# Performance work log

Measured on AMD Instinct MI355X. Metric: run time of the kernel, lower is better.

Reference implementation:

```python
import jax, jax.numpy as jnp
import numpy as np

B, D, H, W, C = 2, 5, 32, 32, 256
NH, NL, NP = 8, 5, 16
HD = C // NH
MLP_H = 4 * C
HW = H * W
LQ = D * HW


def setup_inputs() -> dict:
    key = jax.random.key(0)
    ks = jax.random.split(key, 12)
    s = 0.02
    return {
        "x": jax.random.normal(ks[0], (B, D, H, W, C), jnp.float32),
        "reference_points": jax.random.uniform(ks[1], (B, LQ, NL, 2), jnp.float32),
        "spatial_shapes": np.array([[H, W]] * NL, np.int32),
        "level_start_index": (np.arange(NL) * HW).astype(np.int32),
        "norm3_g": jnp.ones((C,), jnp.float32),
        "norm3_b": jnp.zeros((C,), jnp.float32),
        "norm4_g": jnp.ones((C,), jnp.float32),
        "norm4_b": jnp.zeros((C,), jnp.float32),
        "w_off": jax.random.normal(ks[2], (C, NH * NL * NP * 2), jnp.float32) * s,
        "b_off": jnp.zeros((NH * NL * NP * 2,), jnp.float32),
        "w_attn": jax.random.normal(ks[3], (C, NH * NL * NP), jnp.float32) * s,
        "b_attn": jnp.zeros((NH * NL * NP,), jnp.float32),
        "w_val": jax.random.normal(ks[4], (C, C), jnp.float32) * s,
        "b_val": jnp.zeros((C,), jnp.float32),
        "w_out": jax.random.normal(ks[5], (C, C), jnp.float32) * s,
        "b_out": jnp.zeros((C,), jnp.float32),
        "w_fc1": jax.random.normal(ks[6], (C, MLP_H), jnp.float32) * s,
        "b_fc1": jnp.zeros((MLP_H,), jnp.float32),
        "w_fc2": jax.random.normal(ks[7], (MLP_H, C), jnp.float32) * s,
        "b_fc2": jnp.zeros((C,), jnp.float32),
    }


def _ln(x, g, b, eps=1e-5):
    m = x.mean(-1, keepdims=True)
    v = ((x - m) ** 2).mean(-1, keepdims=True)
    return (x - m) * jax.lax.rsqrt(v + eps) * g + b


def _msdeform(q, ref, w_off, b_off, w_attn, b_attn, w_val, b_val, w_out, b_out):
    """Standard Deformable-DETR MSDeformAttn; self-attention (value = query input)."""
    Bq = q.shape[0]
    val = (q @ w_val + b_val).reshape(Bq, LQ, NH, HD)
    off = (q @ w_off + b_off).reshape(Bq, LQ, NH, NL, NP, 2)
    aw = jax.nn.softmax((q @ w_attn + b_attn).reshape(Bq, LQ, NH, NL * NP), axis=-1)
    aw = aw.reshape(Bq, LQ, NH, NL, NP)
    # offset normalizer: (W, H) per level (all levels HxW here)
    loc = ref[:, :, None, :, None, :] + off / jnp.array([W, H], jnp.float32)
    out = jnp.zeros((Bq, LQ, NH, HD), jnp.float32)
    for l in range(NL):  # loop over 5 levels (structural, small)
        vl = val[:, l * HW:(l + 1) * HW].transpose(0, 2, 1, 3).reshape(Bq * NH, HW, HD)
        ll = loc[:, :, :, l].transpose(0, 2, 1, 3, 4)  # [B, NH, LQ, NP, 2]
        # grid_sample align_corners=False, grid = 2*loc - 1 => pixel = loc*size - 0.5
        px = ll[..., 0] * W - 0.5
        py = ll[..., 1] * H - 0.5
        x0 = jnp.floor(px)
        y0 = jnp.floor(py)
        fx = px - x0
        fy = py - y0
        x0i = x0.astype(jnp.int32)
        y0i = y0.astype(jnp.int32)
        samp = jnp.zeros((Bq * NH, LQ * NP, HD), jnp.float32)
        for dy, dx, wgt in ((0, 0, (1 - fy) * (1 - fx)), (0, 1, (1 - fy) * fx),
                            (1, 0, fy * (1 - fx)), (1, 1, fy * fx)):
            xi = x0i + dx
            yi = y0i + dy
            valid = ((xi >= 0) & (xi < W) & (yi >= 0) & (yi < H)).astype(jnp.float32)
            idx = (jnp.clip(yi, 0, H - 1) * W + jnp.clip(xi, 0, W - 1)).reshape(Bq * NH, LQ * NP, 1)
            g = jnp.take_along_axis(vl, idx, axis=1)  # [B*NH, LQ*NP, HD]
            samp = samp + g * (wgt * valid).reshape(Bq * NH, LQ * NP, 1)
        samp = samp.reshape(Bq, NH, LQ, NP, HD)
        out = out + jnp.einsum('bqhp,bhqpd->bqhd', aw[:, :, :, l], samp)
    return out.reshape(Bq, LQ, C) @ w_out + b_out


def reference(x, reference_points, spatial_shapes, level_start_index,
              norm3_g, norm3_b, norm4_g, norm4_b,
              w_off, b_off, w_attn, b_attn, w_val, b_val, w_out, b_out,
              w_fc1, b_fc1, w_fc2, b_fc2):
    # forward_part3: norm3 -> flatten -> MSDeformAttn (D == 5, no padding path)
    q = _ln(x, norm3_g, norm3_b).reshape(B, LQ, C)
    attn = _msdeform(q, reference_points, w_off, b_off, w_attn, b_attn,
                     w_val, b_val, w_out, b_out)
    x = x + attn.reshape(B, D, H, W, C)  # shortcut + drop_path(identity)
    # forward_part4: norm4 -> MLP (GELU, exact) residual
    h = _ln(x, norm4_g, norm4_b)
    m = jax.nn.gelu(h @ w_fc1 + b_fc1, approximate=False) @ w_fc2 + b_fc2
    return x + m
```

## Files before the change

kernel.cpp:

```cpp
#include <hip/hip_runtime.h>
#include <hip/hip_bf16.h>
#include <math.h>

#define B_   2
#define D_   5
#define H_   32
#define W_   32
#define C_   256
#define NH_  8
#define NL_  5
#define NP_  16
#define HD_  32
#define HW_  1024
#define LQ_  5120
#define M_   (B_*LQ_)
#define MLP_ 1024
#define NCAT 2176

typedef unsigned short u16;
typedef __bf16 bf16x8 __attribute__((ext_vector_type(8)));
typedef float  f32x4  __attribute__((ext_vector_type(4)));
typedef float  f32x2  __attribute__((ext_vector_type(2)));

__device__ __forceinline__ float b2f(u16 v) {
    union { float f; unsigned u; } x; x.u = ((unsigned)v) << 16; return x.f;
}
__device__ __forceinline__ u16 f2b(float f) {
    union { float f; unsigned u; } x; x.f = f;
    unsigned r = x.u + 0x7fffu + ((x.u >> 16) & 1u);
    return (u16)(r >> 16);
}
__device__ __forceinline__ void gload16(const u16* g, u16* l) {
    __builtin_amdgcn_global_load_lds(
        (const __attribute__((address_space(1))) unsigned int*)g,
        (__attribute__((address_space(3))) unsigned int*)l, 16, 0, 0);
}

#define SEG0 557056
#define SEG1 622592
#define SEG2 884736
#define SEG3 1146880
#define SEGT 1149056
__global__ void prep_weights(const float* __restrict__ w_val, const float* __restrict__ w_off,
                             const float* __restrict__ w_attn, const float* __restrict__ w_out,
                             const float* __restrict__ w_fc1, const float* __restrict__ w_fc2,
                             const float* __restrict__ b_val, const float* __restrict__ b_off,
                             const float* __restrict__ b_attn,
                             u16* __restrict__ wcatT, u16* __restrict__ woutT,
                             u16* __restrict__ wfc1T, u16* __restrict__ wfc2T,
                             float* __restrict__ biascat) {
    int idx = blockIdx.x * blockDim.x + threadIdx.x;
    if (idx < SEG0) {
        int n = idx >> 8, k = idx & 255;
        float v;
        if (n < 256)        v = w_val[k * 256 + n];
        else if (n < 1536)  v = w_off[k * 1280 + (n - 256)];
        else                v = w_attn[k * 640 + (n - 1536)];
        wcatT[idx] = f2b(v);
    } else if (idx < SEG1) {
        int i = idx - SEG0; int n = i >> 8, k = i & 255;
        woutT[i] = f2b(w_out[k * 256 + n]);
    } else if (idx < SEG2) {
        int i = idx - SEG1; int n = i >> 8, k = i & 255;
        wfc1T[i] = f2b(w_fc1[k * 1024 + n]);
    } else if (idx < SEG3) {
        int i = idx - SEG2; int n = i >> 10, k = i & 1023;
        wfc2T[i] = f2b(w_fc2[k * 256 + n]);
    } else if (idx < SEGT) {
        int t = idx - SEG3;
        float v;
        if (t < 256)        v = b_val[t];
        else if (t < 1536)  v = b_off[t - 256];
        else                v = b_attn[t - 1536];
        biascat[t] = v;
    }
}

__global__ void ln_rows(const float* __restrict__ x, const float* __restrict__ g,
                        const float* __restrict__ b, u16* __restrict__ out) {
    int wave = threadIdx.x >> 6, lane = threadIdx.x & 63;
    int row = blockIdx.x * 4 + wave;
    const float4 v = *(const float4*)(x + (size_t)row * C_ + lane * 4);
    float s = v.x + v.y + v.z + v.w;
#pragma unroll
    for (int o = 1; o < 64; o <<= 1) s += __shfl_xor(s, o, 64);
    float mean = s * (1.0f / C_);
    float4 d = { v.x - mean, v.y - mean, v.z - mean, v.w - mean };
    float s2 = d.x * d.x + d.y * d.y + d.z * d.z + d.w * d.w;
#pragma unroll
    for (int o = 1; o < 64; o <<= 1) s2 += __shfl_xor(s2, o, 64);
    float r = rsqrtf(s2 * (1.0f / C_) + 1e-5f);
    const float4 gg = *(const float4*)(g + lane * 4);
    const float4 bb = *(const float4*)(b + lane * 4);
    unsigned lo = (unsigned)f2b(d.x * r * gg.x + bb.x) |
                  ((unsigned)f2b(d.y * r * gg.y + bb.y) << 16);
    unsigned hi = (unsigned)f2b(d.z * r * gg.z + bb.z) |
                  ((unsigned)f2b(d.w * r * gg.w + bb.w) << 16);
    uint2 pk = { lo, hi };
    *(uint2*)(out + (size_t)row * C_ + lane * 4) = pk;
}

#define BK 64
__launch_bounds__(256, 2)
__global__ void gemm128(const u16* __restrict__ A, const u16* __restrict__ Bt,
                        const float* __restrict__ bias,
                        void* __restrict__ out, int Mdim, int Ndim, int Kdim,
                        int mode, int nTiles) {
    __shared__ __align__(16) u16 lsA[128 * BK];
    __shared__ __align__(16) u16 lsB[128 * BK];
    int bm = blockIdx.x / nTiles, bn = blockIdx.x % nTiles;
    int m0 = bm * 128, n0 = bn * 128;
    int tid = threadIdx.x;
    int lane = tid & 63, wv = tid >> 6;
    int quad = lane >> 4, l16 = lane & 15;
    int rw = (wv >> 1) * 64, cw = (wv & 1) * 64;

    f32x4 acc[4][4];
#pragma unroll
    for (int i = 0; i < 4; i++)
#pragma unroll
        for (int j = 0; j < 4; j++) { f32x4 z = {0.f, 0.f, 0.f, 0.f}; acc[i][j] = z; }

    for (int k0 = 0; k0 < Kdim; k0 += BK) {
        __syncthreads();
#pragma unroll
        for (int s = 0; s < 4; s++) {
            int cc = s * 256 + wv * 64 + lane;
            int row = cc >> 3, kc = (cc & 7) << 3;
            int lbase = (s * 256 + wv * 64) * 8;
            gload16(A  + (size_t)(m0 + row) * Kdim + k0 + kc, &lsA[lbase]);
            gload16(Bt + (size_t)(n0 + row) * Kdim + k0 + kc, &lsB[lbase]);
        }
        __syncthreads();
#pragma unroll
        for (int kk = 0; kk < 2; kk++) {
            bf16x8 af[4], bfr[4];
#pragma unroll
            for (int i = 0; i < 4; i++)
                af[i] = *(const bf16x8*)(&lsA[(rw + i * 16 + l16) * BK + kk * 32 + quad * 8]);
#pragma unroll
            for (int j = 0; j < 4; j++)
                bfr[j] = *(const bf16x8*)(&lsB[(cw + j * 16 + l16) * BK + kk * 32 + quad * 8]);
#pragma unroll
            for (int i = 0; i < 4; i++)
#pragma unroll
                for (int j = 0; j < 4; j++)
                    acc[i][j] = __builtin_amdgcn_mfma_f32_16x16x32_bf16(
                        af[i], bfr[j], acc[i][j], 0, 0, 0);
        }
    }

#pragma unroll
    for (int i = 0; i < 4; i++) {
#pragma unroll
        for (int j = 0; j < 4; j++) {
            int col = n0 + cw + j * 16 + l16;
            float bb = bias[col];
#pragma unroll
            for (int r = 0; r < 4; r++) {
                int row = m0 + rw + i * 16 + quad * 4 + r;
                float v = acc[i][j][r] + bb;
                size_t off = (size_t)row * Ndim + col;
                if (mode == 0) {
                    ((u16*)out)[off] = f2b(v);
                } else {
                    float t = 0.5f * v * (1.0f + erff(v * 0.70710678f));
                    ((u16*)out)[off] = f2b(t);
                }
            }
        }
    }
}

__launch_bounds__(256, 4)
__global__ void gemm64_res(const u16* __restrict__ A, const u16* __restrict__ Bt,
                           const float* __restrict__ bias, const float* __restrict__ res,
                           float* __restrict__ out, int Mdim, int Ndim, int Kdim,
                           int nTiles) {
    __shared__ __align__(16) u16 lsA[64 * BK];
    __shared__ __align__(16) u16 lsB[128 * BK];
    int bm = blockIdx.x / nTiles, bn = blockIdx.x % nTiles;
    int m0 = bm * 64, n0 = bn * 128;
    int tid = threadIdx.x;
    int lane = tid & 63, wv = tid >> 6;
    int quad = lane >> 4, l16 = lane & 15;
    int rw = wv * 16;

    f32x4 acc[8];
#pragma unroll
    for (int j = 0; j < 8; j++) { f32x4 z = {0.f, 0.f, 0.f, 0.f}; acc[j] = z; }

    for (int k0 = 0; k0 < Kdim; k0 += BK) {
        __syncthreads();
#pragma unroll
        for (int s = 0; s < 2; s++) {
            int cc = s * 256 + wv * 64 + lane;
            int row = cc >> 3, kc = (cc & 7) << 3;
            int lbase = (s * 256 + wv * 64) * 8;
            gload16(A + (size_t)(m0 + row) * Kdim + k0 + kc, &lsA[lbase]);
        }
#pragma unroll
        for (int s = 0; s < 4; s++) {
            int cc = s * 256 + wv * 64 + lane;
            int row = cc >> 3, kc = (cc & 7) << 3;
            int lbase = (s * 256 + wv * 64) * 8;
            gload16(Bt + (size_t)(n0 + row) * Kdim + k0 + kc, &lsB[lbase]);
        }
        __syncthreads();
#pragma unroll
        for (int kk = 0; kk < 2; kk++) {
            bf16x8 af, bfr[8];
            af = *(const bf16x8*)(&lsA[(rw + l16) * BK + kk * 32 + quad * 8]);
#pragma unroll
            for (int j = 0; j < 8; j++)
                bfr[j] = *(const bf16x8*)(&lsB[(j * 16 + l16) * BK + kk * 32 + quad * 8]);
#pragma unroll
            for (int j = 0; j < 8; j++)
                acc[j] = __builtin_amdgcn_mfma_f32_16x16x32_bf16(
                    af, bfr[j], acc[j], 0, 0, 0);
        }
    }

#pragma unroll
    for (int j = 0; j < 8; j++) {
        int col = n0 + j * 16 + l16;
        float bb = bias[col];
#pragma unroll
        for (int r = 0; r < 4; r++) {
            int row = m0 + rw + quad * 4 + r;
            size_t off = (size_t)row * Ndim + col;
            out[off] = acc[j][r] + bb + res[off];
        }
    }
}

#define SPC 84
__launch_bounds__(256, 2)
__global__ void msdeform_sample(const u16* __restrict__ qkv,
                                const float* __restrict__ ref,
                                u16* __restrict__ outp) {
    __shared__ int2 sparam[NH_ * 4 * SPC];
    int m = blockIdx.x;
    int b = m / LQ_;
    int tid = threadIdx.x;
    int g = tid >> 5;
    int lane = tid & 31;

    const u16* logit_base = qkv + (size_t)m * NCAT + 1536 + g * 80;
    const u16* off_base   = qkv + (size_t)m * NCAT + 256  + g * 160;

    float lv[3];
    float lmax = -1e30f;
    {
        int c = 0;
        for (int i = lane; i < 80; i += 32, c++) {
            lv[c] = b2f(logit_base[i]);
            lmax = fmaxf(lmax, lv[c]);
        }
    }
#pragma unroll
    for (int o = 16; o > 0; o >>= 1) lmax = fmaxf(lmax, __shfl_xor(lmax, o, 32));
    float lsum = 0.f;
    {
        int c = 0;
        for (int i = lane; i < 80; i += 32, c++) {
            lv[c] = __expf(lv[c] - lmax);
            lsum += lv[c];
        }
    }
#pragma unroll
    for (int o = 16; o > 0; o >>= 1) lsum += __shfl_xor(lsum, o, 32);
    float inv = 1.0f / lsum;

    {
        int c = 0;
        for (int i = lane; i < 80; i += 32, c++) {
            float aw = lv[c] * inv;
            int l = i >> 4, p = i & 15;
            float rx = ref[((size_t)m * NL_ + l) * 2 + 0];
            float ry = ref[((size_t)m * NL_ + l) * 2 + 1];
            float ox = b2f(off_base[l * 32 + p * 2 + 0]);
            float oy = b2f(off_base[l * 32 + p * 2 + 1]);
            float px = rx * (float)W_ + ox - 0.5f;
            float py = ry * (float)H_ + oy - 0.5f;
            float x0 = floorf(px), y0 = floorf(py);
            float fx = px - x0, fy = py - y0;
            int x0i = (int)x0, y0i = (int)y0;
            int rowbase = b * LQ_ + l * HW_;
            int sbase = g * 4 * SPC + i;
#pragma unroll
            for (int cc = 0; cc < 4; cc++) {
                int dy = cc >> 1, dx = cc & 1;
                int xi = x0i + dx, yi = y0i + dy;
                float wgt = (dy ? fy : 1.f - fy) * (dx ? fx : 1.f - fx);
                bool valid = (xi >= 0) && (xi < W_) && (yi >= 0) && (yi < H_);
                int xc = min(max(xi, 0), W_ - 1);
                int yc = min(max(yi, 0), H_ - 1);
                int boff = (((rowbase + yc * W_ + xc) * NCAT) + g * 32) * 2;
                float w = valid ? wgt * aw : 0.f;
                int2 pk = { boff, __float_as_int(w) };
                sparam[sbase + cc * SPC] = pk;
            }
        }
    }
    __syncthreads();

    const char* qb = (const char*)qkv;
    int c4 = lane >> 3;
    int s2 = (lane >> 2) & 1;
    int chq = lane & 3;
    int pbase = g * 4 * SPC + c4 * SPC + s2;
    int laneoff = chq * 16;
    f32x2 p0 = {0.f, 0.f}, p1 = {0.f, 0.f}, p2 = {0.f, 0.f}, p3 = {0.f, 0.f};
#pragma unroll 8
    for (int i = 0; i < 40; i++) {
        int2 p = sparam[pbase + i * 2];
        f32x2 w2; w2.x = __int_as_float(p.y); w2.y = w2.x;
        unsigned voff = (unsigned)(p.x + laneoff);
        uint4 v = *(const uint4*)(qb + voff);
        union { unsigned u[2]; f32x2 f; } c0, c1, c2, c3;
        c0.u[0] = v.x << 16; c0.u[1] = v.x & 0xffff0000u;
        c1.u[0] = v.y << 16; c1.u[1] = v.y & 0xffff0000u;
        c2.u[0] = v.z << 16; c2.u[1] = v.z & 0xffff0000u;
        c3.u[0] = v.w << 16; c3.u[1] = v.w & 0xffff0000u;
        p0 += w2 * c0.f;
        p1 += w2 * c1.f;
        p2 += w2 * c2.f;
        p3 += w2 * c3.f;
    }
    float a0 = p0.x, a1 = p0.y, a2 = p1.x, a3 = p1.y;
    float a4 = p2.x, a5 = p2.y, a6 = p3.x, a7 = p3.y;
#pragma unroll
    for (int o = 4; o <= 16; o <<= 1) {
        a0 += __shfl_xor(a0, o, 32); a1 += __shfl_xor(a1, o, 32);
        a2 += __shfl_xor(a2, o, 32); a3 += __shfl_xor(a3, o, 32);
        a4 += __shfl_xor(a4, o, 32); a5 += __shfl_xor(a5, o, 32);
        a6 += __shfl_xor(a6, o, 32); a7 += __shfl_xor(a7, o, 32);
    }
    if (lane < 4) {
        uint4 pk;
        pk.x = (unsigned)f2b(a0) | ((unsigned)f2b(a1) << 16);
        pk.y = (unsigned)f2b(a2) | ((unsigned)f2b(a3) << 16);
        pk.z = (unsigned)f2b(a4) | ((unsigned)f2b(a5) << 16);
        pk.w = (unsigned)f2b(a6) | ((unsigned)f2b(a7) << 16);
        *(uint4*)(outp + (size_t)m * C_ + g * 32 + chq * 8) = pk;
    }
}

extern "C" void kernel_launch(void* const* d_in, const int* in_sizes, int n_in,
                              void* d_out, int out_size, void* d_ws, size_t ws_size,
                              hipStream_t stream) {
    const float* x      = (const float*)d_in[0];
    const float* ref    = (const float*)d_in[1];
    const float* n3g    = (const float*)d_in[4];
    const float* n3b    = (const float*)d_in[5];
    const float* n4g    = (const float*)d_in[6];
    const float* n4b    = (const float*)d_in[7];
    const float* w_off  = (const float*)d_in[8];
    const float* b_off  = (const float*)d_in[9];
    const float* w_attn = (const float*)d_in[10];
    const float* b_attn = (const float*)d_in[11];
    const float* w_val  = (const float*)d_in[12];
    const float* b_val  = (const float*)d_in[13];
    const float* w_out  = (const float*)d_in[14];
    const float* b_out  = (const float*)d_in[15];
    const float* w_fc1  = (const float*)d_in[16];
    const float* b_fc1  = (const float*)d_in[17];
    const float* w_fc2  = (const float*)d_in[18];
    const float* b_fc2  = (const float*)d_in[19];
    float* out = (float*)d_out;

    u16*   wcatT   = (u16*)d_ws;
    float* biascat = (float*)(wcatT + (size_t)NCAT * 256);
    u16*   woutT   = (u16*)(biascat + 2304);
    u16*   wfc1T   = woutT + 256 * 256;
    u16*   wfc2T   = wfc1T + 1024 * 256;
    u16*   qbuf    = wfc2T + 256 * 1024;
    u16*   qkv     = qbuf + (size_t)M_ * 256;
    u16*   outp    = qkv + (size_t)M_ * NCAT;
    float* x2      = (float*)qkv;
    u16*   hbuf    = (u16*)(x2 + (size_t)M_ * 256);
    u16*   gbuf    = hbuf + (size_t)M_ * 256;

    prep_weights<<<dim3((SEGT + 255) / 256), dim3(256), 0, stream>>>(
        w_val, w_off, w_attn, w_out, w_fc1, w_fc2, b_val, b_off, b_attn,
        wcatT, woutT, wfc1T, wfc2T, biascat);

    ln_rows<<<dim3(M_ / 4), dim3(256), 0, stream>>>(x, n3g, n3b, qbuf);

    gemm128<<<dim3(80 * 17), dim3(256), 0, stream>>>(
        qbuf, wcatT, biascat, qkv, M_, NCAT, 256, 0, 17);

    msdeform_sample<<<dim3(M_), dim3(256), 0, stream>>>(qkv, ref, outp);

    gemm64_res<<<dim3(160 * 2), dim3(256), 0, stream>>>(
        outp, woutT, b_out, x, x2, M_, 256, 256, 2);

    ln_rows<<<dim3(M_ / 4), dim3(256), 0, stream>>>(x2, n4g, n4b, hbuf);

    gemm128<<<dim3(80 * 8), dim3(256), 0, stream>>>(
        hbuf, wfc1T, b_fc1, gbuf, M_, 1024, 256, 1, 8);

    gemm64_res<<<dim3(160 * 2), dim3(256), 0, stream>>>(
        gbuf, wfc2T, b_fc2, x2, out, M_, 256, 1024, 2);
}
```

Baseline: 282.7 us.

## Store value projection head-major and fuse output projection with second LayerNorm

The fused projection GEMM now writes the value columns into a separate head-major buffer [B*NH, LQ, 32], so bilinear gathers in the sampling kernel read contiguous 64-byte rows instead of strided rows of the wide concatenated buffer. The remaining offset and logit columns go to a narrower buffer. A new kernel fuses the output projection, the residual add and the norm4 LayerNorm using a full-width 32-row tile, which removes one launch and a round trip of x2. The sampling inner loop is also rewritten with scalar accumulators and a smaller unroll. The cost is scattered epilogue stores in the GEMM and a single-pass variance formula in the fused LayerNorm.

```diff
diff --git a/kernel.cpp b/kernel.cpp
--- a/kernel.cpp
+++ b/kernel.cpp
@@ -16,11 +16,11 @@
 #define M_   (B_*LQ_)
 #define MLP_ 1024
 #define NCAT 2176
+#define NQ2  1920
 
 typedef unsigned short u16;
 typedef __bf16 bf16x8 __attribute__((ext_vector_type(8)));
 typedef float  f32x4  __attribute__((ext_vector_type(4)));
-typedef float  f32x2  __attribute__((ext_vector_type(2)));
 
 __device__ __forceinline__ float b2f(u16 v) {
     union { float f; unsigned u; } x; x.u = ((unsigned)v) << 16; return x.f;
@@ -104,7 +104,8 @@
 __launch_bounds__(256, 2)
 __global__ void gemm128(const u16* __restrict__ A, const u16* __restrict__ Bt,
                         const float* __restrict__ bias,
-                        void* __restrict__ out, int Mdim, int Ndim, int Kdim,
+                        u16* __restrict__ out, u16* __restrict__ valT,
+                        int Mdim, int Ndim, int Kdim,
                         int mode, int nTiles) {
     __shared__ __align__(16) u16 lsA[128 * BK];
     __shared__ __align__(16) u16 lsB[128 * BK];
@@ -160,15 +161,106 @@
             for (int r = 0; r < 4; r++) {
                 int row = m0 + rw + i * 16 + quad * 4 + r;
                 float v = acc[i][j][r] + bb;
-                size_t off = (size_t)row * Ndim + col;
                 if (mode == 0) {
-                    ((u16*)out)[off] = f2b(v);
+                    if (col < 256) {
+                        int b2 = row >= LQ_;
+                        int pix = row - b2 * LQ_;
+                        int h = col >> 5, ch = col & 31;
+                        valT[(((size_t)(b2 * NH_ + h) * LQ_) + pix) * 32 + ch] = f2b(v);
+                    } else {
+                        out[(size_t)row * NQ2 + (col - 256)] = f2b(v);
+                    }
                 } else {
                     float t = 0.5f * v * (1.0f + erff(v * 0.70710678f));
-                    ((u16*)out)[off] = f2b(t);
+                    out[(size_t)row * Ndim + col] = f2b(t);
                 }
             }
         }
+    }
+}
+
+__launch_bounds__(256, 2)
+__global__ void gemm_wout_ln(const u16* __restrict__ A, const u16* __restrict__ Bt,
+                             const float* __restrict__ bias, const float* __restrict__ res,
+                             const float* __restrict__ g4, const float* __restrict__ b4,
+                             float* __restrict__ x2, u16* __restrict__ hb) {
+    __shared__ __align__(16) u16 lsA[32 * BK];
+    __shared__ __align__(16) u16 lsB[256 * BK];
+    int m0 = blockIdx.x * 32;
+    int tid = threadIdx.x;
+    int lane = tid & 63, wv = tid >> 6;
+    int quad = lane >> 4, l16 = lane & 15;
+    int r0 = (wv & 1) * 16, c0 = (wv >> 1) * 128;
+
+    f32x4 acc[8];
+#pragma unroll
+    for (int j = 0; j < 8; j++) { f32x4 z = {0.f, 0.f, 0.f, 0.f}; acc[j] = z; }
+
+    for (int k0 = 0; k0 < 256; k0 += BK) {
+        __syncthreads();
+        {
+            int cc = wv * 64 + lane;
+            int row = cc >> 3, kc = (cc & 7) << 3;
+            gload16(A + (size_t)(m0 + row) * 256 + k0 + kc, &lsA[(wv * 64) * 8]);
+        }
+#pragma unroll
+        for (int s = 0; s < 8; s++) {
+            int cc = s * 256 + wv * 64 + lane;
+            int row = cc >> 3, kc = (cc & 7) << 3;
+            gload16(Bt + (size_t)row * 256 + k0 + kc, &lsB[(s * 256 + wv * 64) * 8]);
+        }
+        __syncthreads();
+#pragma unroll
+        for (int kk = 0; kk < 2; kk++) {
+            bf16x8 af, bfr[8];
+            af = *(const bf16x8*)(&lsA[(r0 + l16) * BK + kk * 32 + quad * 8]);
+#pragma unroll
+            for (int j = 0; j < 8; j++)
+                bfr[j] = *(const bf16x8*)(&lsB[(c0 + j * 16 + l16) * BK + kk * 32 + quad * 8]);
+#pragma unroll
+            for (int j = 0; j < 8; j++)
+                acc[j] = __builtin_amdgcn_mfma_f32_16x16x32_bf16(af, bfr[j], acc[j], 0, 0, 0);
+        }
+    }
+
+    __syncthreads();
+    float* tile = (float*)lsB;
+#pragma unroll
+    for (int j = 0; j < 8; j++) {
+        int col = c0 + j * 16 + l16;
+        float bb = bias[col];
+#pragma unroll
+        for (int r = 0; r < 4; r++) {
+            int rl = r0 + quad * 4 + r;
+            int row = m0 + rl;
+            float v = acc[j][r] + bb + res[(size_t)row * C_ + col];
+            tile[rl * 256 + col] = v;
+            x2[(size_t)row * C_ + col] = v;
+        }
+    }
+    __syncthreads();
+    const float4 gg = *(const float4*)(g4 + lane * 4);
+    const float4 bv = *(const float4*)(b4 + lane * 4);
+#pragma unroll
+    for (int rr = 0; rr < 8; rr++) {
+        int rl = wv * 8 + rr;
+        float4 v = *(const float4*)(&tile[rl * 256 + lane * 4]);
+        float s = v.x + v.y + v.z + v.w;
+        float s2 = v.x * v.x + v.y * v.y + v.z * v.z + v.w * v.w;
+#pragma unroll
+        for (int o = 1; o < 64; o <<= 1) {
+            s  += __shfl_xor(s, o, 64);
+            s2 += __shfl_xor(s2, o, 64);
+        }
+        float mean = s * (1.0f / C_);
+        float var = s2 * (1.0f / C_) - mean * mean;
+        float rstd = rsqrtf(var + 1e-5f);
+        unsigned lo = (unsigned)f2b((v.x - mean) * rstd * gg.x + bv.x) |
+                      ((unsigned)f2b((v.y - mean) * rstd * gg.y + bv.y) << 16);
+        unsigned hi = (unsigned)f2b((v.z - mean) * rstd * gg.z + bv.z) |
+                      ((unsigned)f2b((v.w - mean) * rstd * gg.w + bv.w) << 16);
+        uint2 pk = { lo, hi };
+        *(uint2*)(hb + (size_t)(m0 + rl) * C_ + lane * 4) = pk;
     }
 }
 
@@ -196,15 +288,13 @@
         for (int s = 0; s < 2; s++) {
             int cc = s * 256 + wv * 64 + lane;
             int row = cc >> 3, kc = (cc & 7) << 3;
-            int lbase = (s * 256 + wv * 64) * 8;
-            gload16(A + (size_t)(m0 + row) * Kdim + k0 + kc, &lsA[lbase]);
+            gload16(A + (size_t)(m0 + row) * Kdim + k0 + kc, &lsA[(s * 256 + wv * 64) * 8]);
         }
 #pragma unroll
         for (int s = 0; s < 4; s++) {
             int cc = s * 256 + wv * 64 + lane;
             int row = cc >> 3, kc = (cc & 7) << 3;
-            int lbase = (s * 256 + wv * 64) * 8;
-            gload16(Bt + (size_t)(n0 + row) * Kdim + k0 + kc, &lsB[lbase]);
+            gload16(Bt + (size_t)(n0 + row) * Kdim + k0 + kc, &lsB[(s * 256 + wv * 64) * 8]);
         }
         __syncthreads();
 #pragma unroll
@@ -216,8 +306,7 @@
                 bfr[j] = *(const bf16x8*)(&lsB[(j * 16 + l16) * BK + kk * 32 + quad * 8]);
 #pragma unroll
             for (int j = 0; j < 8; j++)
-                acc[j] = __builtin_amdgcn_mfma_f32_16x16x32_bf16(
-                    af, bfr[j], acc[j], 0, 0, 0);
+                acc[j] = __builtin_amdgcn_mfma_f32_16x16x32_bf16(af, bfr[j], acc[j], 0, 0, 0);
         }
     }
 
@@ -236,7 +325,8 @@
 
 #define SPC 84
 __launch_bounds__(256, 2)
-__global__ void msdeform_sample(const u16* __restrict__ qkv,
+__global__ void msdeform_sample(const u16* __restrict__ qkv2,
+                                const u16* __restrict__ valT,
                                 const float* __restrict__ ref,
                                 u16* __restrict__ outp) {
     __shared__ int2 sparam[NH_ * 4 * SPC];
@@ -246,8 +336,8 @@
     int g = tid >> 5;
     int lane = tid & 31;
 
-    const u16* logit_base = qkv + (size_t)m * NCAT + 1536 + g * 80;
-    const u16* off_base   = qkv + (size_t)m * NCAT + 256  + g * 160;
+    const u16* logit_base = qkv2 + (size_t)m * NQ2 + 1280 + g * 80;
+    const u16* off_base   = qkv2 + (size_t)m * NQ2 + g * 160;
 
     float lv[3];
     float lmax = -1e30f;
@@ -286,7 +376,7 @@
             float x0 = floorf(px), y0 = floorf(py);
             float fx = px - x0, fy = py - y0;
             int x0i = (int)x0, y0i = (int)y0;
-            int rowbase = b * LQ_ + l * HW_;
+            int hbase = (b * NH_ + g) * LQ_ + l * HW_;
             int sbase = g * 4 * SPC + i;
 #pragma unroll
             for (int cc = 0; cc < 4; cc++) {
@@ -296,7 +386,7 @@
                 bool valid = (xi >= 0) && (xi < W_) && (yi >= 0) && (yi < H_);
                 int xc = min(max(xi, 0), W_ - 1);
                 int yc = min(max(yi, 0), H_ - 1);
-                int boff = (((rowbase + yc * W_ + xc) * NCAT) + g * 32) * 2;
+                int boff = (hbase + yc * W_ + xc) * 64;
                 float w = valid ? wgt * aw : 0.f;
                 int2 pk = { boff, __float_as_int(w) };
                 sparam[sbase + cc * SPC] = pk;
@@ -305,31 +395,29 @@
     }
     __syncthreads();
 
-    const char* qb = (const char*)qkv;
+    const char* qb = (const char*)valT;
     int c4 = lane >> 3;
     int s2 = (lane >> 2) & 1;
     int chq = lane & 3;
     int pbase = g * 4 * SPC + c4 * SPC + s2;
     int laneoff = chq * 16;
-    f32x2 p0 = {0.f, 0.f}, p1 = {0.f, 0.f}, p2 = {0.f, 0.f}, p3 = {0.f, 0.f};
-#pragma unroll 8
+    float a0 = 0.f, a1 = 0.f, a2 = 0.f, a3 = 0.f;
+    float a4 = 0.f, a5 = 0.f, a6 = 0.f, a7 = 0.f;
+#pragma unroll 4
     for (int i = 0; i < 40; i++) {
         int2 p = sparam[pbase + i * 2];
-        f32x2 w2; w2.x = __int_as_float(p.y); w2.y = w2.x;
-        unsigned voff = (unsigned)(p.x + laneoff);
-        uint4 v = *(const uint4*)(qb + voff);
-        union { unsigned u[2]; f32x2 f; } c0, c1, c2, c3;
-        c0.u[0] = v.x << 16; c0.u[1] = v.x & 0xffff0000u;
-        c1.u[0] = v.y << 16; c1.u[1] = v.y & 0xffff0000u;
-        c2.u[0] = v.z << 16; c2.u[1] = v.z & 0xffff0000u;
-        c3.u[0] = v.w << 16; c3.u[1] = v.w & 0xffff0000u;
-        p0 += w2 * c0.f;
-        p1 += w2 * c1.f;
-        p2 += w2 * c2.f;
-        p3 += w2 * c3.f;
-    }
-    float a0 = p0.x, a1 = p0.y, a2 = p1.x, a3 = p1.y;
-    float a4 = p2.x, a5 = p2.y, a6 = p3.x, a7 = p3.y;
+        float w = __int_as_float(p.y);
+        uint4 v = *(const uint4*)(qb + p.x + laneoff);
+        union { unsigned u; float f; } t;
+        t.u = v.x << 16;         a0 += w * t.f;
+        t.u = v.x & 0xffff0000u; a1 += w * t.f;
+        t.u = v.y << 16;         a2 += w * t.f;
+        t.u = v.y & 0xffff0000u; a3 += w * t.f;
+        t.u = v.z << 16;         a4 += w * t.f;
+        t.u = v.z & 0xffff0000u; a5 += w * t.f;
+        t.u = v.w << 16;         a6 += w * t.f;
+        t.u = v.w & 0xffff0000u; a7 += w * t.f;
+    }
 #pragma unroll
     for (int o = 4; o <= 16; o <<= 1) {
         a0 += __shfl_xor(a0, o, 32); a1 += __shfl_xor(a1, o, 32);
@@ -376,9 +464,10 @@
     u16*   wfc1T   = woutT + 256 * 256;
     u16*   wfc2T   = wfc1T + 1024 * 256;
     u16*   qbuf    = wfc2T + 256 * 1024;
-    u16*   qkv     = qbuf + (size_t)M_ * 256;
-    u16*   outp    = qkv + (size_t)M_ * NCAT;
-    float* x2      = (float*)qkv;
+    u16*   valT    = qbuf + (size_t)M_ * 256;
+    u16*   qkv2    = valT + (size_t)M_ * 256;
+    u16*   outp    = qkv2 + (size_t)M_ * NQ2;
+    float* x2      = (float*)qkv2;
     u16*   hbuf    = (u16*)(x2 + (size_t)M_ * 256);
     u16*   gbuf    = hbuf + (size_t)M_ * 256;
 
@@ -389,17 +478,15 @@
     ln_rows<<<dim3(M_ / 4), dim3(256), 0, stream>>>(x, n3g, n3b, qbuf);
 
     gemm128<<<dim3(80 * 17), dim3(256), 0, stream>>>(
-        qbuf, wcatT, biascat, qkv, M_, NCAT, 256, 0, 17);
-
-    msdeform_sample<<<dim3(M_), dim3(256), 0, stream>>>(qkv, ref, outp);
-
-    gemm64_res<<<dim3(160 * 2), dim3(256), 0, stream>>>(
-        outp, woutT, b_out, x, x2, M_, 256, 256, 2);
-
-    ln_rows<<<dim3(M_ / 4), dim3(256), 0, stream>>>(x2, n4g, n4b, hbuf);
+        qbuf, wcatT, biascat, qkv2, valT, M_, NCAT, 256, 0, 17);
+
+    msdeform_sample<<<dim3(M_), dim3(256), 0, stream>>>(qkv2, valT, ref, outp);
+
+    gemm_wout_ln<<<dim3(M_ / 32), dim3(256), 0, stream>>>(
+        outp, woutT, b_out, x, n4g, n4b, x2, hbuf);
 
     gemm128<<<dim3(80 * 8), dim3(256), 0, stream>>>(
-        hbuf, wfc1T, b_fc1, gbuf, M_, 1024, 256, 1, 8);
+        hbuf, wfc1T, b_fc1, gbuf, nullptr, M_, 1024, 256, 1, 8);
 
     gemm64_res<<<dim3(160 * 2), dim3(256), 0, stream>>>(
         gbuf, wfc2T, b_fc2, x2, out, M_, 256, 1024, 2);
```

Result: faster. 263.5 us (-6.8%).
